# Optimization experiments

Hardware: AMD Instinct MI355X
Metric: run time of the kernel (lower is better)

Reference implementation:

```python
import jax, jax.numpy as jnp
import numpy as np

N = 50000
E = 800000
D_IN = 256
D_OUT = 256
ALPHA = 0.5


def setup_inputs() -> dict:
    key = jax.random.key(0)
    k1, k2, k3, k4, k5, k6 = jax.random.split(key, 6)
    stdv = 1.0 / np.sqrt(D_OUT)
    return {
        "input": jax.random.normal(k1, (N, D_IN), dtype=jnp.float32),
        "adj_src": jax.random.randint(k2, (E,), 0, N, dtype=jnp.int64),
        "adj_dst": jax.random.randint(k3, (E,), 0, N, dtype=jnp.int64),
        "adj_w": jax.random.uniform(k4, (E,), dtype=jnp.float32),
        "init_input": jax.random.normal(k5, (N, D_OUT), dtype=jnp.float32),
        "weight": jax.random.uniform(k6, (D_IN, D_OUT), dtype=jnp.float32,
                                     minval=-stdv, maxval=stdv),
    }


def reference(input, adj_src, adj_dst, adj_w, init_input, weight):
    # support = input @ W          [N, D_OUT] (dense GEMM)
    support = jnp.matmul(input, weight)
    # spmm: out[dst] += w * support[src]   (COO aggregate)
    msgs = support[adj_src] * adj_w[:, None]          # [E, D_OUT]
    agg = jax.ops.segment_sum(msgs, adj_dst, num_segments=N)  # [N, D_OUT]
    # alpha-blended residual + ReLU (bias=False, act=ReLU)
    out = agg * ALPHA + init_input * (1.0 - ALPHA)
    return jax.nn.relu(out)
```

## Files before the change

### kernel.cpp

```cpp
#include <hip/hip_runtime.h>
#include <hip/hip_fp16.h>

#define ALPHA 0.5f

typedef short short8v __attribute__((ext_vector_type(8)));
typedef float f32x4 __attribute__((ext_vector_type(4)));

__device__ __forceinline__ unsigned short f2bf(float f) {
  union { float f; unsigned u; } v; v.f = f;
  unsigned r = v.u + 0x7FFFu + ((v.u >> 16) & 1u);
  return (unsigned short)(r >> 16);
}
__device__ __forceinline__ float bf2f(unsigned short u) {
  union { unsigned u; float f; } v; v.u = ((unsigned)u) << 16;
  return v.f;
}
__device__ __forceinline__ float unpack_w(unsigned p) {
  return __half2float(__ushort_as_half((unsigned short)((p & 0x7FFFu) << 1)));
}

__global__ __launch_bounds__(256) void prep_small(
    const float* __restrict__ W, unsigned short* __restrict__ Wt,
    int* __restrict__ deg, int* __restrict__ scanmeta, int N) {
  const int tid = threadIdx.x;
  const int bid = blockIdx.x;
  if (bid < 256) {
    __shared__ float tile[16][17];
    const int kb = (bid & 15) * 16, nb = (bid >> 4) * 16;
    const int tx = tid & 15, ty = tid >> 4;
    tile[ty][tx] = W[(kb + ty) * 256 + nb + tx];
    __syncthreads();
    Wt[(nb + ty) * 256 + kb + tx] = f2bf(tile[tx][ty]);
  } else {
    if (bid == 256 && tid < 128) scanmeta[tid] = 0;
    const int base = ((bid - 256) * 256 + tid) * 4;
    if (base + 3 < N) *reinterpret_cast<int4*>(&deg[base]) = make_int4(0, 0, 0, 0);
    else for (int j = 0; j < 4; ++j) if (base + j < N) deg[base + j] = 0;
  }
}

__global__ __launch_bounds__(256) void gemm_hist(
    const float* __restrict__ A, const unsigned short* __restrict__ Wt,
    unsigned short* __restrict__ C, int M,
    const int* __restrict__ dst, int* __restrict__ deg, int E, int GB, int HB) {
  __shared__ char smem[2][24576];
  const int tid = threadIdx.x;
  const int bid = blockIdx.x;

  if (bid >= GB) {
    const int hgid = (bid - GB) * 256 + tid;
    const int hstride = HB * 256;
    const int E4 = E & ~3;
    for (int i = hgid * 4; i < E4; i += hstride * 4) {
      int4 d = *reinterpret_cast<const int4*>(&dst[i]);
      atomicAdd(&deg[d.x], 1); atomicAdd(&deg[d.y], 1);
      atomicAdd(&deg[d.z], 1); atomicAdd(&deg[d.w], 1);
    }
    if (hgid < (E - E4)) atomicAdd(&deg[dst[E4 + hgid]], 1);
    return;
  }

  const int lane = tid & 63;
  const int w = tid >> 6;
  const int wm = w >> 1, wn = w & 1;
  const int row0 = bid * 128;

  f32x4 acc[4][8];
  #pragma unroll
  for (int m = 0; m < 4; ++m)
    #pragma unroll
    for (int n = 0; n < 8; ++n) acc[m][n] = (f32x4){0.f, 0.f, 0.f, 0.f};

  const int aR = tid >> 1;
  const int aKs = (tid & 1) * 16;
  const int aRow = (row0 + aR < M) ? (row0 + aR) : (M - 1);
  const float* aP = A + (size_t)aRow * 256 + aKs;
  const int aWrOff = (aR >> 4) * 1024 + (aKs >> 3) * 256 + (aR & 15) * 16;

  int cur = 0;
  {
    float4 av[4];
    #pragma unroll
    for (int j = 0; j < 4; ++j) av[j] = *reinterpret_cast<const float4*>(aP + j * 4);
    #pragma unroll
    for (int i = 0; i < 4; ++i) {
      int s = w * 4 + i;
      const unsigned short* g = Wt + (size_t)(s * 16 + (lane & 15)) * 256 + (lane >> 4) * 8;
      __builtin_amdgcn_global_load_lds(
          (const __attribute__((address_space(1))) void*)g,
          (__attribute__((address_space(3))) void*)(&smem[0][8192 + s * 1024]),
          16, 0, 0);
    }
    unsigned short ab[16];
    #pragma unroll
    for (int j = 0; j < 4; ++j) {
      ab[j * 4 + 0] = f2bf(av[j].x); ab[j * 4 + 1] = f2bf(av[j].y);
      ab[j * 4 + 2] = f2bf(av[j].z); ab[j * 4 + 3] = f2bf(av[j].w);
    }
    *reinterpret_cast<short8v*>(&smem[0][aWrOff])       = *reinterpret_cast<short8v*>(&ab[0]);
    *reinterpret_cast<short8v*>(&smem[0][aWrOff + 256]) = *reinterpret_cast<short8v*>(&ab[8]);
    __syncthreads();
  }

  #pragma unroll
  for (int t = 0; t < 8; ++t) {
    float4 av[4];
    const bool pf = (t < 7);
    if (pf) {
      const int k0 = (t + 1) * 32;
      #pragma unroll
      for (int j = 0; j < 4; ++j) av[j] = *reinterpret_cast<const float4*>(aP + k0 + j * 4);
      #pragma unroll
      for (int i = 0; i < 4; ++i) {
        int s = w * 4 + i;
        const unsigned short* g = Wt + (size_t)(s * 16 + (lane & 15)) * 256 + k0 + (lane >> 4) * 8;
        __builtin_amdgcn_global_load_lds(
            (const __attribute__((address_space(1))) void*)g,
            (__attribute__((address_space(3))) void*)(&smem[cur ^ 1][8192 + s * 1024]),
            16, 0, 0);
      }
    }
    short8v af[4], bfv[8];
    #pragma unroll
    for (int m = 0; m < 4; ++m)
      af[m] = *reinterpret_cast<const short8v*>(&smem[cur][(wm * 4 + m) * 1024 + lane * 16]);
    #pragma unroll
    for (int n = 0; n < 8; ++n)
      bfv[n] = *reinterpret_cast<const short8v*>(&smem[cur][8192 + (wn * 8 + n) * 1024 + lane * 16]);
    #pragma unroll
    for (int m = 0; m < 4; ++m)
      #pragma unroll
      for (int n = 0; n < 8; ++n)
        acc[m][n] = __builtin_amdgcn_mfma_f32_16x16x32_bf16(af[m], bfv[n], acc[m][n], 0, 0, 0);
    if (pf) {
      unsigned short ab[16];
      #pragma unroll
      for (int j = 0; j < 4; ++j) {
        ab[j * 4 + 0] = f2bf(av[j].x); ab[j * 4 + 1] = f2bf(av[j].y);
        ab[j * 4 + 2] = f2bf(av[j].z); ab[j * 4 + 3] = f2bf(av[j].w);
      }
      *reinterpret_cast<short8v*>(&smem[cur ^ 1][aWrOff])       = *reinterpret_cast<short8v*>(&ab[0]);
      *reinterpret_cast<short8v*>(&smem[cur ^ 1][aWrOff + 256]) = *reinterpret_cast<short8v*>(&ab[8]);
    }
    __syncthreads();
    cur ^= 1;
  }

  #pragma unroll
  for (int m = 0; m < 4; ++m) {
    #pragma unroll
    for (int n = 0; n < 8; ++n) {
      const int col = wn * 128 + n * 16 + (lane & 15);
      #pragma unroll
      for (int r = 0; r < 4; ++r) {
        const int row = row0 + wm * 64 + m * 16 + (lane >> 4) * 4 + r;
        if (row < M) C[(size_t)row * 256 + col] = f2bf(acc[m][n][r]);
      }
    }
  }
}

__global__ __launch_bounds__(256) void scan_lookback(
    const int* __restrict__ deg, int* __restrict__ row_ptr, int* __restrict__ cursor,
    int* __restrict__ scanmeta ,
    int N, int E, int NB) {
  int* flags = scanmeta;
  int* aggv  = scanmeta + 64;
  const int tid = threadIdx.x;
  const int bid = blockIdx.x;
  const int base = bid * 1024 + tid * 4;

  int4 v = make_int4(0, 0, 0, 0);
  if (base + 3 < N) v = *reinterpret_cast<const int4*>(&deg[base]);
  else {
    if (base + 0 < N) v.x = deg[base + 0];
    if (base + 1 < N) v.y = deg[base + 1];
    if (base + 2 < N) v.z = deg[base + 2];
  }
  const int s = v.x + v.y + v.z + v.w;
  const int lane = tid & 63, wid = tid >> 6;
  int ps = s;
  #pragma unroll
  for (int off = 1; off < 64; off <<= 1) {
    int t = __shfl_up(ps, off, 64);
    if (lane >= off) ps += t;
  }
  __shared__ int wsum[4];
  __shared__ int s_off;
  if (lane == 63) wsum[wid] = ps;
  __syncthreads();
  int woff = 0;
  #pragma unroll
  for (int w2 = 0; w2 < 4; ++w2) woff += (w2 < wid) ? wsum[w2] : 0;
  const int texcl = woff + ps - s;

  if (tid == 0) {
    int total = wsum[0] + wsum[1] + wsum[2] + wsum[3];
    atomicExch(&aggv[bid], total);
    __threadfence();
    atomicExch(&flags[bid], 1);
  }
  if (bid == 0 && tid == 0) row_ptr[N] = E;

  if (tid < 64) {
    int a = 0;
    if (tid < bid) {
      while (atomicAdd(&flags[tid], 0) == 0) { }
      a = atomicAdd(&aggv[tid], 0);
    }
    #pragma unroll
    for (int m = 1; m < 64; m <<= 1) a += __shfl_xor(a, m, 64);
    if (tid == 0) s_off = a;
  }
  __syncthreads();
  const int off = s_off;

  int4 e = make_int4(texcl + off, texcl + off + v.x,
                     texcl + off + v.x + v.y, texcl + off + v.x + v.y + v.z);
  if (base + 3 < N) {
    *reinterpret_cast<int4*>(&row_ptr[base]) = e;
    *reinterpret_cast<int4*>(&cursor[base]) = e;
  } else {
    int ev[4] = {e.x, e.y, e.z, e.w};
    for (int j = 0; j < 4; ++j)
      if (base + j < N) { row_ptr[base + j] = ev[j]; cursor[base + j] = ev[j]; }
  }
}

__global__ __launch_bounds__(256) void reindex_edges(
    const int* __restrict__ src, const int* __restrict__ dst,
    const float* __restrict__ w, int* __restrict__ cursor,
    unsigned* __restrict__ edges, int E) {
  int i = (blockIdx.x * blockDim.x + threadIdx.x) * 4;
  if (i + 3 < E) {
    int4 sv = *reinterpret_cast<const int4*>(&src[i]);
    int4 dv = *reinterpret_cast<const int4*>(&dst[i]);
    float4 wv = *reinterpret_cast<const float4*>(&w[i]);
    int s_[4] = {sv.x, sv.y, sv.z, sv.w};
    int d_[4] = {dv.x, dv.y, dv.z, dv.w};
    float w_[4] = {wv.x, wv.y, wv.z, wv.w};
    #pragma unroll
    for (int j = 0; j < 4; ++j) {
      int slot = atomicAdd(&cursor[d_[j]], 1);
      unsigned hb = __half_as_ushort(__float2half(w_[j] * ALPHA));
      edges[slot] = ((unsigned)s_[j] << 15) | (hb >> 1);
    }
  } else {
    for (; i < E; ++i) {
      int slot = atomicAdd(&cursor[dst[i]], 1);
      unsigned hb = __half_as_ushort(__float2half(w[i] * ALPHA));
      edges[slot] = ((unsigned)src[i] << 15) | (hb >> 1);
    }
  }
}

__global__ __launch_bounds__(256) void aggregate(
    const unsigned short* __restrict__ support,
    const int* __restrict__ row_ptr,
    const unsigned* __restrict__ edges,
    const float* __restrict__ init, float* __restrict__ out, int N) {
  int node = blockIdx.x * 4 + (threadIdx.x >> 6);
  if (node >= N) return;
  int lane = threadIdx.x & 63;
  int start = row_ptr[node];
  int cnt = row_ptr[node + 1] - start;

  float4 ini = *reinterpret_cast<const float4*>(&init[(size_t)node * 256 + lane * 4]);

  float4 acc = make_float4(0.f, 0.f, 0.f, 0.f);
  int e = 0;
  for (; e + 7 < cnt; e += 8) {
    unsigned p[8];
    #pragma unroll
    for (int j = 0; j < 8; ++j) p[j] = edges[start + e + j];
    ushort4 v[8];
    #pragma unroll
    for (int j = 0; j < 8; ++j)
      v[j] = *reinterpret_cast<const ushort4*>(&support[(size_t)(p[j] >> 15) * 256 + lane * 4]);
    #pragma unroll
    for (int j = 0; j < 8; ++j) {
      float wj = unpack_w(p[j]);
      acc.x += wj * bf2f(v[j].x);
      acc.y += wj * bf2f(v[j].y);
      acc.z += wj * bf2f(v[j].z);
      acc.w += wj * bf2f(v[j].w);
    }
  }
  for (; e < cnt; ++e) {
    unsigned p = edges[start + e];
    ushort4 v = *reinterpret_cast<const ushort4*>(&support[(size_t)(p >> 15) * 256 + lane * 4]);
    float wj = unpack_w(p);
    acc.x += wj * bf2f(v.x); acc.y += wj * bf2f(v.y);
    acc.z += wj * bf2f(v.z); acc.w += wj * bf2f(v.w);
  }
  float4 o;
  o.x = fmaxf(acc.x + (1.f - ALPHA) * ini.x, 0.f);
  o.y = fmaxf(acc.y + (1.f - ALPHA) * ini.y, 0.f);
  o.z = fmaxf(acc.z + (1.f - ALPHA) * ini.z, 0.f);
  o.w = fmaxf(acc.w + (1.f - ALPHA) * ini.w, 0.f);
  *reinterpret_cast<float4*>(&out[(size_t)node * 256 + lane * 4]) = o;
}

extern "C" void kernel_launch(void* const* d_in, const int* in_sizes, int n_in,
                              void* d_out, int out_size, void* d_ws, size_t ws_size,
                              hipStream_t stream) {
  const float* input   = (const float*)d_in[0];
  const int*   adj_src = (const int*)d_in[1];
  const int*   adj_dst = (const int*)d_in[2];
  const float* adj_w   = (const float*)d_in[3];
  const float* init_in = (const float*)d_in[4];
  const float* weight  = (const float*)d_in[5];
  float* out = (float*)d_out;

  const int N = in_sizes[0] / 256;
  const int E = in_sizes[1];

  char* ws = (char*)d_ws;
  unsigned short* support = (unsigned short*)ws; ws += (size_t)N * 256 * 2;
  unsigned short* Wt      = (unsigned short*)ws; ws += 256 * 256 * 2;
  int* deg      = (int*)ws; ws += (size_t)N * 4;
  int* row_ptr  = (int*)ws; ws += (size_t)(N + 1) * 4;
  int* cursor   = (int*)ws; ws += (size_t)N * 4;
  int* scanmeta = (int*)ws; ws += 128 * 4;
  unsigned* edges = (unsigned*)ws; ws += (size_t)E * 4;

  const int NB = (N + 1023) / 1024;
  const int GB = (N + 127) / 128;
  const int HB = 800;

  prep_small<<<256 + (N / 4 + 255) / 256, 256, 0, stream>>>(weight, Wt, deg, scanmeta, N);

  gemm_hist<<<GB + HB, 256, 0, stream>>>(input, Wt, support, N,
                                         adj_dst, deg, E, GB, HB);

  scan_lookback<<<NB, 256, 0, stream>>>(deg, row_ptr, cursor, scanmeta, N, E, NB);

  reindex_edges<<<(E / 4 + 255) / 256, 256, 0, stream>>>(adj_src, adj_dst, adj_w, cursor, edges, E);

  aggregate<<<(N + 3) / 4, 256, 0, stream>>>(support, row_ptr, edges, init_in, out, N);
}
```

Baseline: 173.7 us.

## Shrink GEMM tiles, put histogram blocks first, fuse scan with edge reindex

The GEMM moves from 128-row double-buffered tiles to 32-row single-buffered tiles with 18 KB of shared memory. This gives many more, smaller blocks for better occupancy and load spread, at the cost of more re-reads of W. Histogram blocks are now placed ahead of GEMM blocks in the grid so they get scheduled first. The scan and edge-reindex kernels become one launch, where reindex blocks spin on a global done counter until all scan blocks finish. That removes a kernel launch boundary but assumes the scan blocks are scheduled before or alongside the spinning blocks, which risks deadlock or wasted cycles.

```diff
diff --git a/kernel.cpp b/kernel.cpp
--- a/kernel.cpp
+++ b/kernel.cpp
@@ -32,7 +32,7 @@
     __syncthreads();
     Wt[(nb + ty) * 256 + kb + tx] = f2bf(tile[tx][ty]);
   } else {
-    if (bid == 256 && tid < 128) scanmeta[tid] = 0;
+    if (bid == 256 && tid < 192) scanmeta[tid] = 0;
     const int base = ((bid - 256) * 256 + tid) * 4;
     if (base + 3 < N) *reinterpret_cast<int4*>(&deg[base]) = make_int4(0, 0, 0, 0);
     else for (int j = 0; j < 4; ++j) if (base + j < N) deg[base + j] = 0;
@@ -42,13 +42,12 @@
 __global__ __launch_bounds__(256) void gemm_hist(
     const float* __restrict__ A, const unsigned short* __restrict__ Wt,
     unsigned short* __restrict__ C, int M,
-    const int* __restrict__ dst, int* __restrict__ deg, int E, int GB, int HB) {
-  __shared__ char smem[2][24576];
+    const int* __restrict__ dst, int* __restrict__ deg, int E, int HB, int GB) {
   const int tid = threadIdx.x;
   const int bid = blockIdx.x;
 
-  if (bid >= GB) {
-    const int hgid = (bid - GB) * 256 + tid;
+  if (bid < HB) {
+    const int hgid = bid * 256 + tid;
     const int hstride = HB * 256;
     const int E4 = E & ~3;
     for (int i = hgid * 4; i < E4; i += hstride * 4) {
@@ -60,182 +59,156 @@
     return;
   }
 
+  __shared__ char smem[18432];
+  const int gb = bid - HB;
+  const int row0 = gb * 32;
   const int lane = tid & 63;
   const int w = tid >> 6;
-  const int wm = w >> 1, wn = w & 1;
-  const int row0 = bid * 128;
-
-  f32x4 acc[4][8];
+
+  f32x4 acc[2][4];
   #pragma unroll
-  for (int m = 0; m < 4; ++m)
-    #pragma unroll
-    for (int n = 0; n < 8; ++n) acc[m][n] = (f32x4){0.f, 0.f, 0.f, 0.f};
-
-  const int aR = tid >> 1;
-  const int aKs = (tid & 1) * 16;
-  const int aRow = (row0 + aR < M) ? (row0 + aR) : (M - 1);
-  const float* aP = A + (size_t)aRow * 256 + aKs;
-  const int aWrOff = (aR >> 4) * 1024 + (aKs >> 3) * 256 + (aR & 15) * 16;
-
-  int cur = 0;
-  {
-    float4 av[4];
-    #pragma unroll
-    for (int j = 0; j < 4; ++j) av[j] = *reinterpret_cast<const float4*>(aP + j * 4);
+  for (int m = 0; m < 2; ++m)
+    #pragma unroll
+    for (int n = 0; n < 4; ++n) acc[m][n] = (f32x4){0.f, 0.f, 0.f, 0.f};
+
+  const int aR = tid >> 3;
+  const int aK4 = (tid & 7) * 4;
+  int rr = row0 + aR;
+  const int aRow = (rr < M) ? rr : (M - 1);
+  const float* aP = A + (size_t)aRow * 256 + aK4;
+  const int aOff = (aR >> 4) * 1024 + (aK4 >> 3) * 256 + (aR & 15) * 16 + ((aK4 & 7) ? 8 : 0);
+
+  #pragma unroll
+  for (int t = 0; t < 8; ++t) {
+    if (t) __syncthreads();
+    const int k0 = t * 32;
     #pragma unroll
     for (int i = 0; i < 4; ++i) {
       int s = w * 4 + i;
-      const unsigned short* g = Wt + (size_t)(s * 16 + (lane & 15)) * 256 + (lane >> 4) * 8;
+      const unsigned short* g = Wt + (size_t)(s * 16 + (lane & 15)) * 256 + k0 + (lane >> 4) * 8;
       __builtin_amdgcn_global_load_lds(
           (const __attribute__((address_space(1))) void*)g,
-          (__attribute__((address_space(3))) void*)(&smem[0][8192 + s * 1024]),
+          (__attribute__((address_space(3))) void*)(&smem[2048 + s * 1024]),
           16, 0, 0);
     }
-    unsigned short ab[16];
-    #pragma unroll
-    for (int j = 0; j < 4; ++j) {
-      ab[j * 4 + 0] = f2bf(av[j].x); ab[j * 4 + 1] = f2bf(av[j].y);
-      ab[j * 4 + 2] = f2bf(av[j].z); ab[j * 4 + 3] = f2bf(av[j].w);
-    }
-    *reinterpret_cast<short8v*>(&smem[0][aWrOff])       = *reinterpret_cast<short8v*>(&ab[0]);
-    *reinterpret_cast<short8v*>(&smem[0][aWrOff + 256]) = *reinterpret_cast<short8v*>(&ab[8]);
-    __syncthreads();
+    float4 av = *reinterpret_cast<const float4*>(aP + k0);
+    unsigned short ab[4] = {f2bf(av.x), f2bf(av.y), f2bf(av.z), f2bf(av.w)};
+    *reinterpret_cast<uint2*>(&smem[aOff]) = *reinterpret_cast<uint2*>(ab);
+    __syncthreads();
+    short8v af[2], bfv[4];
+    #pragma unroll
+    for (int m = 0; m < 2; ++m)
+      af[m] = *reinterpret_cast<const short8v*>(&smem[m * 1024 + lane * 16]);
+    #pragma unroll
+    for (int n = 0; n < 4; ++n)
+      bfv[n] = *reinterpret_cast<const short8v*>(&smem[2048 + (w * 4 + n) * 1024 + lane * 16]);
+    #pragma unroll
+    for (int m = 0; m < 2; ++m)
+      #pragma unroll
+      for (int n = 0; n < 4; ++n)
+        acc[m][n] = __builtin_amdgcn_mfma_f32_16x16x32_bf16(af[m], bfv[n], acc[m][n], 0, 0, 0);
   }
 
   #pragma unroll
-  for (int t = 0; t < 8; ++t) {
-    float4 av[4];
-    const bool pf = (t < 7);
-    if (pf) {
-      const int k0 = (t + 1) * 32;
+  for (int m = 0; m < 2; ++m) {
+    #pragma unroll
+    for (int n = 0; n < 4; ++n) {
+      const int col = w * 64 + n * 16 + (lane & 15);
       #pragma unroll
-      for (int j = 0; j < 4; ++j) av[j] = *reinterpret_cast<const float4*>(aP + k0 + j * 4);
-      #pragma unroll
-      for (int i = 0; i < 4; ++i) {
-        int s = w * 4 + i;
-        const unsigned short* g = Wt + (size_t)(s * 16 + (lane & 15)) * 256 + k0 + (lane >> 4) * 8;
-        __builtin_amdgcn_global_load_lds(
-            (const __attribute__((address_space(1))) void*)g,
-            (__attribute__((address_space(3))) void*)(&smem[cur ^ 1][8192 + s * 1024]),
-            16, 0, 0);
+      for (int r2 = 0; r2 < 4; ++r2) {
+        const int row = row0 + m * 16 + (lane >> 4) * 4 + r2;
+        if (row < M) C[(size_t)row * 256 + col] = f2bf(acc[m][n][r2]);
       }
     }
-    short8v af[4], bfv[8];
-    #pragma unroll
-    for (int m = 0; m < 4; ++m)
-      af[m] = *reinterpret_cast<const short8v*>(&smem[cur][(wm * 4 + m) * 1024 + lane * 16]);
-    #pragma unroll
-    for (int n = 0; n < 8; ++n)
-      bfv[n] = *reinterpret_cast<const short8v*>(&smem[cur][8192 + (wn * 8 + n) * 1024 + lane * 16]);
-    #pragma unroll
-    for (int m = 0; m < 4; ++m)
-      #pragma unroll
-      for (int n = 0; n < 8; ++n)
-        acc[m][n] = __builtin_amdgcn_mfma_f32_16x16x32_bf16(af[m], bfv[n], acc[m][n], 0, 0, 0);
-    if (pf) {
-      unsigned short ab[16];
-      #pragma unroll
-      for (int j = 0; j < 4; ++j) {
-        ab[j * 4 + 0] = f2bf(av[j].x); ab[j * 4 + 1] = f2bf(av[j].y);
-        ab[j * 4 + 2] = f2bf(av[j].z); ab[j * 4 + 3] = f2bf(av[j].w);
-      }
-      *reinterpret_cast<short8v*>(&smem[cur ^ 1][aWrOff])       = *reinterpret_cast<short8v*>(&ab[0]);
-      *reinterpret_cast<short8v*>(&smem[cur ^ 1][aWrOff + 256]) = *reinterpret_cast<short8v*>(&ab[8]);
-    }
-    __syncthreads();
-    cur ^= 1;
-  }
-
-  #pragma unroll
-  for (int m = 0; m < 4; ++m) {
-    #pragma unroll
-    for (int n = 0; n < 8; ++n) {
-      const int col = wn * 128 + n * 16 + (lane & 15);
-      #pragma unroll
-      for (int r = 0; r < 4; ++r) {
-        const int row = row0 + wm * 64 + m * 16 + (lane >> 4) * 4 + r;
-        if (row < M) C[(size_t)row * 256 + col] = f2bf(acc[m][n][r]);
-      }
-    }
-  }
-}
-
-__global__ __launch_bounds__(256) void scan_lookback(
+  }
+}
+
+__global__ __launch_bounds__(256) void scan_reindex(
     const int* __restrict__ deg, int* __restrict__ row_ptr, int* __restrict__ cursor,
     int* __restrict__ scanmeta ,
+    const int* __restrict__ src, const int* __restrict__ dst,
+    const float* __restrict__ wgt, unsigned* __restrict__ edges,
     int N, int E, int NB) {
   int* flags = scanmeta;
   int* aggv  = scanmeta + 64;
+  int* done  = scanmeta + 128;
   const int tid = threadIdx.x;
   const int bid = blockIdx.x;
-  const int base = bid * 1024 + tid * 4;
-
-  int4 v = make_int4(0, 0, 0, 0);
-  if (base + 3 < N) v = *reinterpret_cast<const int4*>(&deg[base]);
-  else {
-    if (base + 0 < N) v.x = deg[base + 0];
-    if (base + 1 < N) v.y = deg[base + 1];
-    if (base + 2 < N) v.z = deg[base + 2];
-  }
-  const int s = v.x + v.y + v.z + v.w;
-  const int lane = tid & 63, wid = tid >> 6;
-  int ps = s;
-  #pragma unroll
-  for (int off = 1; off < 64; off <<= 1) {
-    int t = __shfl_up(ps, off, 64);
-    if (lane >= off) ps += t;
-  }
-  __shared__ int wsum[4];
-  __shared__ int s_off;
-  if (lane == 63) wsum[wid] = ps;
+
+  if (bid < NB) {
+    const int base = bid * 1024 + tid * 4;
+    int4 v = make_int4(0, 0, 0, 0);
+    if (base + 3 < N) v = *reinterpret_cast<const int4*>(&deg[base]);
+    else {
+      if (base + 0 < N) v.x = deg[base + 0];
+      if (base + 1 < N) v.y = deg[base + 1];
+      if (base + 2 < N) v.z = deg[base + 2];
+    }
+    const int s = v.x + v.y + v.z + v.w;
+    const int lane = tid & 63, wid = tid >> 6;
+    int ps = s;
+    #pragma unroll
+    for (int off = 1; off < 64; off <<= 1) {
+      int t = __shfl_up(ps, off, 64);
+      if (lane >= off) ps += t;
+    }
+    __shared__ int wsum[4];
+    __shared__ int s_off;
+    if (lane == 63) wsum[wid] = ps;
+    __syncthreads();
+    int woff = 0;
+    #pragma unroll
+    for (int w2 = 0; w2 < 4; ++w2) woff += (w2 < wid) ? wsum[w2] : 0;
+    const int texcl = woff + ps - s;
+
+    if (tid == 0) {
+      int total = wsum[0] + wsum[1] + wsum[2] + wsum[3];
+      atomicExch(&aggv[bid], total);
+      __threadfence();
+      atomicExch(&flags[bid], 1);
+    }
+    if (bid == 0 && tid == 0) row_ptr[N] = E;
+
+    if (tid < 64) {
+      int a = 0;
+      if (tid < bid) {
+        while (atomicAdd(&flags[tid], 0) == 0) { }
+        a = atomicAdd(&aggv[tid], 0);
+      }
+      #pragma unroll
+      for (int m = 1; m < 64; m <<= 1) a += __shfl_xor(a, m, 64);
+      if (tid == 0) s_off = a;
+    }
+    __syncthreads();
+    const int off = s_off;
+
+    int4 e = make_int4(texcl + off, texcl + off + v.x,
+                       texcl + off + v.x + v.y, texcl + off + v.x + v.y + v.z);
+    if (base + 3 < N) {
+      *reinterpret_cast<int4*>(&row_ptr[base]) = e;
+      *reinterpret_cast<int4*>(&cursor[base]) = e;
+    } else {
+      int ev[4] = {e.x, e.y, e.z, e.w};
+      for (int j = 0; j < 4; ++j)
+        if (base + j < N) { row_ptr[base + j] = ev[j]; cursor[base + j] = ev[j]; }
+    }
+    __threadfence();
+    __syncthreads();
+    if (tid == 0) atomicAdd(done, 1);
+    return;
+  }
+
+  if (tid == 0) {
+    while (atomicAdd(done, 0) < NB) { }
+  }
   __syncthreads();
-  int woff = 0;
-  #pragma unroll
-  for (int w2 = 0; w2 < 4; ++w2) woff += (w2 < wid) ? wsum[w2] : 0;
-  const int texcl = woff + ps - s;
-
-  if (tid == 0) {
-    int total = wsum[0] + wsum[1] + wsum[2] + wsum[3];
-    atomicExch(&aggv[bid], total);
-    __threadfence();
-    atomicExch(&flags[bid], 1);
-  }
-  if (bid == 0 && tid == 0) row_ptr[N] = E;
-
-  if (tid < 64) {
-    int a = 0;
-    if (tid < bid) {
-      while (atomicAdd(&flags[tid], 0) == 0) { }
-      a = atomicAdd(&aggv[tid], 0);
-    }
-    #pragma unroll
-    for (int m = 1; m < 64; m <<= 1) a += __shfl_xor(a, m, 64);
-    if (tid == 0) s_off = a;
-  }
-  __syncthreads();
-  const int off = s_off;
-
-  int4 e = make_int4(texcl + off, texcl + off + v.x,
-                     texcl + off + v.x + v.y, texcl + off + v.x + v.y + v.z);
-  if (base + 3 < N) {
-    *reinterpret_cast<int4*>(&row_ptr[base]) = e;
-    *reinterpret_cast<int4*>(&cursor[base]) = e;
-  } else {
-    int ev[4] = {e.x, e.y, e.z, e.w};
-    for (int j = 0; j < 4; ++j)
-      if (base + j < N) { row_ptr[base + j] = ev[j]; cursor[base + j] = ev[j]; }
-  }
-}
-
-__global__ __launch_bounds__(256) void reindex_edges(
-    const int* __restrict__ src, const int* __restrict__ dst,
-    const float* __restrict__ w, int* __restrict__ cursor,
-    unsigned* __restrict__ edges, int E) {
-  int i = (blockIdx.x * blockDim.x + threadIdx.x) * 4;
+  __threadfence();
+  const int rbid = bid - NB;
+  int i = (rbid * 256 + tid) * 4;
   if (i + 3 < E) {
     int4 sv = *reinterpret_cast<const int4*>(&src[i]);
     int4 dv = *reinterpret_cast<const int4*>(&dst[i]);
-    float4 wv = *reinterpret_cast<const float4*>(&w[i]);
+    float4 wv = *reinterpret_cast<const float4*>(&wgt[i]);
     int s_[4] = {sv.x, sv.y, sv.z, sv.w};
     int d_[4] = {dv.x, dv.y, dv.z, dv.w};
     float w_[4] = {wv.x, wv.y, wv.z, wv.w};
@@ -248,7 +221,7 @@
   } else {
     for (; i < E; ++i) {
       int slot = atomicAdd(&cursor[dst[i]], 1);
-      unsigned hb = __half_as_ushort(__float2half(w[i] * ALPHA));
+      unsigned hb = __half_as_ushort(__float2half(wgt[i] * ALPHA));
       edges[slot] = ((unsigned)src[i] << 15) | (hb >> 1);
     }
   }
@@ -321,21 +294,21 @@
   int* deg      = (int*)ws; ws += (size_t)N * 4;
   int* row_ptr  = (int*)ws; ws += (size_t)(N + 1) * 4;
   int* cursor   = (int*)ws; ws += (size_t)N * 4;
-  int* scanmeta = (int*)ws; ws += 128 * 4;
+  int* scanmeta = (int*)ws; ws += 192 * 4;
   unsigned* edges = (unsigned*)ws; ws += (size_t)E * 4;
 
   const int NB = (N + 1023) / 1024;
-  const int GB = (N + 127) / 128;
   const int HB = 800;
+  const int GB = (N + 31) / 32;
+  const int RB = (E / 4 + 255) / 256;
 
   prep_small<<<256 + (N / 4 + 255) / 256, 256, 0, stream>>>(weight, Wt, deg, scanmeta, N);
 
-  gemm_hist<<<GB + HB, 256, 0, stream>>>(input, Wt, support, N,
-                                         adj_dst, deg, E, GB, HB);
-
-  scan_lookback<<<NB, 256, 0, stream>>>(deg, row_ptr, cursor, scanmeta, N, E, NB);
-
-  reindex_edges<<<(E / 4 + 255) / 256, 256, 0, stream>>>(adj_src, adj_dst, adj_w, cursor, edges, E);
+  gemm_hist<<<HB + GB, 256, 0, stream>>>(input, Wt, support, N,
+                                         adj_dst, deg, E, HB, GB);
+
+  scan_reindex<<<NB + RB, 256, 0, stream>>>(deg, row_ptr, cursor, scanmeta,
+                                            adj_src, adj_dst, adj_w, edges, N, E, NB);
 
   aggregate<<<(N + 3) / 4, 256, 0, stream>>>(support, row_ptr, edges, init_in, out, N);
 }
```

Result: slower. 242.1 us (+39.3%).
